# Performance work log

Measured on AMD Instinct MI355X. Metric: run time of the kernel, lower is better.

Reference implementation:

```python
import jax, jax.numpy as jnp
import numpy as np

ALPHA = 0.2  # LeakyReLU negative slope


def setup_inputs() -> dict:
    key = jax.random.key(0)
    k1, k2, k3, k4 = jax.random.split(key, 4)
    B, N, F_in, F_out = 2, 512, 256, 128
    x = jax.random.normal(k1, (B, N, F_in), dtype=jnp.float32)
    adj = jax.random.randint(k2, (B, N, N), 0, 2, dtype=jnp.int32)
    # xavier_uniform with gain=1.414 for W (in_features, out_features)
    limit = 1.414 * np.sqrt(6.0 / (F_in + F_out))
    W = jax.random.uniform(k3, (F_in, F_out), dtype=jnp.float32, minval=-limit, maxval=limit)
    # attn_fc: Linear(out_features, 1, bias=False); store its weight as a vector
    lim_a = np.sqrt(1.0 / F_out)
    a_fc = jax.random.uniform(k4, (F_out,), dtype=jnp.float32, minval=-lim_a, maxval=lim_a)
    return {"x": x, "adj": adj, "W": W, "a_fc": a_fc}


def reference(x, adj, W, a_fc):
    # x: [B,N,F_in], adj: [B,N,N], W: [F_in,F_out], a_fc: [F_out]
    Wh = jnp.einsum('bnf,fo->bno', x, W)                         # [B,N,O]
    s = Wh[:, :, None, :] + Wh[:, None, :, :]                    # [B,N,N,O] broadcast concat-sum
    e = jnp.einsum('bijo,o->bij', jax.nn.leaky_relu(s, ALPHA), a_fc)  # attn_fc -> [B,N,N]
    e = e / jnp.sqrt(jnp.sum(e * e))                             # torch.linalg.norm over whole tensor
    e = jnp.where(adj == 0, -jnp.inf, e)
    attention = jax.nn.softmax(e, axis=-1)
    h_prime = jnp.einsum('bij,bjo->bio', attention, Wh)          # [B,N,O]
    return jax.nn.elu(h_prime)                                   # concat=True -> elu
```

## Files before the change

kernel.cpp:

```cpp
#include <hip/hip_runtime.h>
#include <math.h>

constexpr int BB   = 2;
constexpr int NN   = 512;
constexpr int FIN  = 256;
constexpr int FOUT = 128;

__global__ __launch_bounds__(256) void wh_u_kernel(const float* __restrict__ x,
                                                   const float* __restrict__ W,
                                                   const float* __restrict__ a_fc,
                                                   float* __restrict__ Wh,
                                                   float* __restrict__ u2) {
    __shared__ float  xs[4 * FIN];
    __shared__ float4 part[4][16][17];

    const int t  = threadIdx.x;
    const int rg = blockIdx.x & 255;
    const int oh = blockIdx.x >> 8;
    const int g0 = rg * 4;

    ((float4*)xs)[t] = ((const float4*)(x + (size_t)g0 * FIN))[t];
    __syncthreads();

    const int og = t & 15;
    const int fs = t >> 4;
    const float* xr = xs + fs * 16;
    const float4* W4 = (const float4*)W;
    const int ob = oh * 16 + og;

    float4 a0 = {0.f,0.f,0.f,0.f}, a1 = {0.f,0.f,0.f,0.f};
    float4 a2 = {0.f,0.f,0.f,0.f}, a3 = {0.f,0.f,0.f,0.f};
#pragma unroll
    for (int f = 0; f < 16; ++f) {
        const float4 wv = W4[(size_t)(fs * 16 + f) * 32 + ob];
        const float v0 = xr[f];
        const float v1 = xr[FIN + f];
        const float v2 = xr[2 * FIN + f];
        const float v3 = xr[3 * FIN + f];
        a0.x = fmaf(v0, wv.x, a0.x); a1.x = fmaf(v1, wv.x, a1.x);
        a2.x = fmaf(v2, wv.x, a2.x); a3.x = fmaf(v3, wv.x, a3.x);
        a0.y = fmaf(v0, wv.y, a0.y); a1.y = fmaf(v1, wv.y, a1.y);
        a2.y = fmaf(v2, wv.y, a2.y); a3.y = fmaf(v3, wv.y, a3.y);
        a0.z = fmaf(v0, wv.z, a0.z); a1.z = fmaf(v1, wv.z, a1.z);
        a2.z = fmaf(v2, wv.z, a2.z); a3.z = fmaf(v3, wv.z, a3.z);
        a0.w = fmaf(v0, wv.w, a0.w); a1.w = fmaf(v1, wv.w, a1.w);
        a2.w = fmaf(v2, wv.w, a2.w); a3.w = fmaf(v3, wv.w, a3.w);
    }
    part[0][fs][og] = a0;
    part[1][fs][og] = a1;
    part[2][fs][og] = a2;
    part[3][fs][og] = a3;
    __syncthreads();

    if (t < 64) {
        const int rl = t >> 4;
        const int o4 = t & 15;
        float4 s = {0.f, 0.f, 0.f, 0.f};
#pragma unroll
        for (int k = 0; k < 16; ++k) {
            const float4 pk = part[rl][k][o4];
            s.x += pk.x; s.y += pk.y; s.z += pk.z; s.w += pk.w;
        }
        ((float4*)(Wh + (size_t)(g0 + rl) * FOUT))[oh * 16 + o4] = s;

        const float4 a4 = ((const float4*)a_fc)[oh * 16 + o4];
        float pa = s.x * a4.x + s.y * a4.y + s.z * a4.z + s.w * a4.w;
        pa += __shfl_down(pa, 8, 16);
        pa += __shfl_down(pa, 4, 16);
        pa += __shfl_down(pa, 2, 16);
        pa += __shfl_down(pa, 1, 16);
        if (o4 == 0) u2[(size_t)oh * 1024 + g0 + rl] = pa;
    }
}

__global__ __launch_bounds__(256) void e_kernel(const float* __restrict__ Wh,
                                                const float* __restrict__ u2,
                                                const float* __restrict__ a_fc,
                                                float* __restrict__ e_buf,
                                                float* __restrict__ partials) {
    __shared__ float whi[32][132];
    __shared__ float whj[16][132];
    __shared__ float a2[FOUT];
    __shared__ float usi[32];
    __shared__ float usj[16];
    __shared__ float parts[16][4][33];
    __shared__ float red[4];

    const int t   = threadIdx.x;
    const int bj0 = blockIdx.x * 16;
    const int bi0 = blockIdx.y * 32;
    const int b   = blockIdx.z;
    const float* whb = Wh + (size_t)(b * NN) * FOUT;

#pragma unroll
    for (int it = 0; it < 4; ++it) {
        const int idx = it * 256 + t;
        const int row = idx >> 5, c4 = idx & 31;
        *(float4*)&whi[row][c4 * 4] =
            *(const float4*)(whb + (size_t)(bi0 + row) * FOUT + c4 * 4);
    }
#pragma unroll
    for (int it = 0; it < 2; ++it) {
        const int idx = it * 256 + t;
        const int row = idx >> 5, c4 = idx & 31;
        *(float4*)&whj[row][c4 * 4] =
            *(const float4*)(whb + (size_t)(bj0 + row) * FOUT + c4 * 4);
    }
    if (t < 32)
        usi[t] = u2[b * NN + bi0 + t] + u2[1024 + b * NN + bi0 + t];
    else if (t < 48)
        usj[t - 32] = u2[b * NN + bj0 + (t - 32)] +
                      u2[1024 + b * NN + bj0 + (t - 32)];
    else if (t >= 128)
        a2[t - 128] = 0.4f * a_fc[t - 128];
    __syncthreads();

    const int w    = t >> 6;
    const int lane = t & 63;
    const int i    = lane & 31;
    const int jh   = lane >> 5;
    const int ob   = w * 32;

    float4 iv[8], av[8];
#pragma unroll
    for (int k = 0; k < 8; ++k) {
        iv[k] = *(const float4*)&whi[i][ob + 4 * k];
        av[k] = *(const float4*)&a2[ob + 4 * k];
    }

#pragma unroll
    for (int jj = 0; jj < 8; ++jj) {
        const int j = jh * 8 + jj;
        float4 acc = {0.f, 0.f, 0.f, 0.f};
#pragma unroll
        for (int k = 0; k < 8; ++k) {
            const float4 jv = *(const float4*)&whj[j][ob + 4 * k];
            float s;
            s = iv[k].x + jv.x; acc.x = fmaf(av[k].x, fabsf(s), acc.x);
            s = iv[k].y + jv.y; acc.y = fmaf(av[k].y, fabsf(s), acc.y);
            s = iv[k].z + jv.z; acc.z = fmaf(av[k].z, fabsf(s), acc.z);
            s = iv[k].w + jv.w; acc.w = fmaf(av[k].w, fabsf(s), acc.w);
        }
        parts[j][w][i] = (acc.x + acc.y) + (acc.z + acc.w);
    }
    __syncthreads();

    const int ci = t >> 3;
    const int jp = (t & 7) * 2;
    const float ui = usi[ci];

    const float S0 = (parts[jp][0][ci] + parts[jp][1][ci]) +
                     (parts[jp][2][ci] + parts[jp][3][ci]);
    const float v0 = fmaf(0.6f, ui + usj[jp], S0);
    const float S1 = (parts[jp + 1][0][ci] + parts[jp + 1][1][ci]) +
                     (parts[jp + 1][2][ci] + parts[jp + 1][3][ci]);
    const float v1 = fmaf(0.6f, ui + usj[jp + 1], S1);
    float ss = fmaf(v0, v0, v1 * v1);

    float2 e2 = {v0, v1};
    *(float2*)&e_buf[(size_t)(b * NN + bi0 + ci) * NN + bj0 + jp] = e2;

#pragma unroll
    for (int off = 32; off; off >>= 1) ss += __shfl_down(ss, off);
    if ((t & 63) == 0) red[t >> 6] = ss;
    __syncthreads();
    if (t == 0)
        partials[(blockIdx.z * 16 + blockIdx.y) * 32 + blockIdx.x] =
            (red[0] + red[1]) + (red[2] + red[3]);
}

__global__ __launch_bounds__(256) void softmax_pv_kernel(
        const float* __restrict__ e_buf, const int* __restrict__ adj,
        const float* __restrict__ Wh, const float* __restrict__ partials,
        float* __restrict__ out) {
    __shared__ float p[4][NN];
    __shared__ float hb[8][4][32];
    __shared__ float red[4];
    __shared__ float rsv[4];

    const int t    = threadIdx.x;
    const int w    = t >> 6;
    const int lane = t & 63;

    float v = (partials[t] + partials[t + 256]) +
              (partials[t + 512] + partials[t + 768]);
#pragma unroll
    for (int off = 32; off; off >>= 1) v += __shfl_down(v, off);
    if (lane == 0) red[w] = v;
    __syncthreads();
    const float inv_norm = 1.0f / sqrtf((red[0] + red[1]) + (red[2] + red[3]));

    const int g0  = (blockIdx.x & 255) * 4;
    const int oq  = blockIdx.x >> 8;
    const int row = g0 + w;

    const float4* er4 = (const float4*)(e_buf + (size_t)row * NN);
    const int4*   ad4 = (const int4*)(adj + (size_t)row * NN);
    const float4 ea = er4[lane],     eb = er4[lane + 64];
    const int4   aa = ad4[lane],     ab = ad4[lane + 64];

    float va[8];
    va[0] = aa.x ? ea.x * inv_norm : -INFINITY;
    va[1] = aa.y ? ea.y * inv_norm : -INFINITY;
    va[2] = aa.z ? ea.z * inv_norm : -INFINITY;
    va[3] = aa.w ? ea.w * inv_norm : -INFINITY;
    va[4] = ab.x ? eb.x * inv_norm : -INFINITY;
    va[5] = ab.y ? eb.y * inv_norm : -INFINITY;
    va[6] = ab.z ? eb.z * inv_norm : -INFINITY;
    va[7] = ab.w ? eb.w * inv_norm : -INFINITY;

    float mx = va[0];
#pragma unroll
    for (int c = 1; c < 8; ++c) mx = fmaxf(mx, va[c]);
#pragma unroll
    for (int off = 32; off; off >>= 1) mx = fmaxf(mx, __shfl_xor(mx, off));

    float pv[8], sum = 0.f;
#pragma unroll
    for (int c = 0; c < 8; ++c) { pv[c] = expf(va[c] - mx); sum += pv[c]; }
    float4 pa = {pv[0], pv[1], pv[2], pv[3]};
    float4 pb = {pv[4], pv[5], pv[6], pv[7]};
    ((float4*)&p[w][0])[lane]      = pa;
    ((float4*)&p[w][0])[lane + 64] = pb;

#pragma unroll
    for (int off = 32; off; off >>= 1) sum += __shfl_xor(sum, off);
    if (lane == 0) rsv[w] = 1.0f / sum;
    __syncthreads();

    const int oo = lane & 31;
    const int o  = oq * 32 + oo;
    const int jc = (w << 1) | (lane >> 5);
    const int b  = g0 >> 9;
    const float* whb = Wh + (size_t)(b * NN) * FOUT;
    const int j0 = jc * 64;

    float acc0 = 0.f, acc1 = 0.f, acc2 = 0.f, acc3 = 0.f;
    for (int j = j0; j < j0 + 64; j += 4) {
        const float4 p0 = *(const float4*)&p[0][j];
        const float4 p1 = *(const float4*)&p[1][j];
        const float4 p2 = *(const float4*)&p[2][j];
        const float4 p3 = *(const float4*)&p[3][j];
        float wv;
        wv = whb[(size_t)(j + 0) * FOUT + o];
        acc0 = fmaf(p0.x, wv, acc0); acc1 = fmaf(p1.x, wv, acc1);
        acc2 = fmaf(p2.x, wv, acc2); acc3 = fmaf(p3.x, wv, acc3);
        wv = whb[(size_t)(j + 1) * FOUT + o];
        acc0 = fmaf(p0.y, wv, acc0); acc1 = fmaf(p1.y, wv, acc1);
        acc2 = fmaf(p2.y, wv, acc2); acc3 = fmaf(p3.y, wv, acc3);
        wv = whb[(size_t)(j + 2) * FOUT + o];
        acc0 = fmaf(p0.z, wv, acc0); acc1 = fmaf(p1.z, wv, acc1);
        acc2 = fmaf(p2.z, wv, acc2); acc3 = fmaf(p3.z, wv, acc3);
        wv = whb[(size_t)(j + 3) * FOUT + o];
        acc0 = fmaf(p0.w, wv, acc0); acc1 = fmaf(p1.w, wv, acc1);
        acc2 = fmaf(p2.w, wv, acc2); acc3 = fmaf(p3.w, wv, acc3);
    }

    hb[jc][0][oo] = acc0;
    hb[jc][1][oo] = acc1;
    hb[jc][2][oo] = acc2;
    hb[jc][3][oo] = acc3;
    __syncthreads();

    if (t < 128) {
        const int r  = t >> 5;
        const int o2 = t & 31;
        float h = ((hb[0][r][o2] + hb[1][r][o2]) + (hb[2][r][o2] + hb[3][r][o2])) +
                  ((hb[4][r][o2] + hb[5][r][o2]) + (hb[6][r][o2] + hb[7][r][o2]));
        h *= rsv[r];
        out[(size_t)(g0 + r) * FOUT + oq * 32 + o2] = (h > 0.f) ? h : expm1f(h);
    }
}

extern "C" void kernel_launch(void* const* d_in, const int* in_sizes, int n_in,
                              void* d_out, int out_size, void* d_ws, size_t ws_size,
                              hipStream_t stream) {
    const float* x    = (const float*)d_in[0];
    const int*   adj  = (const int*)d_in[1];
    const float* W    = (const float*)d_in[2];
    const float* a_fc = (const float*)d_in[3];
    float* out = (float*)d_out;

    float* ws       = (float*)d_ws;
    float* Wh       = ws;
    float* u2       = ws + 131072;
    float* partials = ws + 131072 + 2048;
    float* e_buf    = ws + 131072 + 2048 + 1024;

    wh_u_kernel<<<dim3(512), dim3(256), 0, stream>>>(x, W, a_fc, Wh, u2);
    e_kernel<<<dim3(NN / 16, NN / 32, BB), dim3(256), 0, stream>>>(Wh, u2, a_fc, e_buf, partials);
    softmax_pv_kernel<<<dim3(1024), dim3(256), 0, stream>>>(e_buf, adj, Wh, partials, out);
}
```

Baseline: 24.63 us.

## Exploit symmetry of attention logits by computing only upper-triangular tiles

```diff
diff --git a/kernel.cpp b/kernel.cpp
--- a/kernel.cpp
+++ b/kernel.cpp
@@ -78,95 +78,94 @@
                                                 const float* __restrict__ a_fc,
                                                 float* __restrict__ e_buf,
                                                 float* __restrict__ partials) {
-    __shared__ float whi[32][132];
+    __shared__ float whi[16][132];
     __shared__ float whj[16][132];
-    __shared__ float a2[FOUT];
-    __shared__ float usi[32];
+    __shared__ float a2s[FOUT];
+    __shared__ float usi[16];
     __shared__ float usj[16];
-    __shared__ float parts[16][4][33];
+    __shared__ float parts[16][4][17];
     __shared__ float red[4];
 
-    const int t   = threadIdx.x;
-    const int bj0 = blockIdx.x * 16;
-    const int bi0 = blockIdx.y * 32;
-    const int b   = blockIdx.z;
+    const int t = threadIdx.x;
+    int s = blockIdx.x;
+    int b = 0;
+    if (s >= 528) { b = 1; s -= 528; }
+    int I = (int)(32.5f - sqrtf(1056.25f - 2.0f * (float)s));
+    int PI = 32 * I - (I * (I - 1)) / 2;
+    if (s < PI)                 { --I; PI = 32 * I - (I * (I - 1)) / 2; }
+    else if (s >= PI + 32 - I)  { PI += 32 - I; ++I; }
+    const int J    = I + (s - PI);
+    const int bi0  = I * 16, bj0 = J * 16;
+    const bool mir = (J > I);
+
     const float* whb = Wh + (size_t)(b * NN) * FOUT;
 
 #pragma unroll
-    for (int it = 0; it < 4; ++it) {
+    for (int it = 0; it < 2; ++it) {
         const int idx = it * 256 + t;
         const int row = idx >> 5, c4 = idx & 31;
         *(float4*)&whi[row][c4 * 4] =
             *(const float4*)(whb + (size_t)(bi0 + row) * FOUT + c4 * 4);
-    }
-#pragma unroll
-    for (int it = 0; it < 2; ++it) {
-        const int idx = it * 256 + t;
-        const int row = idx >> 5, c4 = idx & 31;
         *(float4*)&whj[row][c4 * 4] =
             *(const float4*)(whb + (size_t)(bj0 + row) * FOUT + c4 * 4);
     }
-    if (t < 32)
+    if (t < 16)
         usi[t] = u2[b * NN + bi0 + t] + u2[1024 + b * NN + bi0 + t];
-    else if (t < 48)
-        usj[t - 32] = u2[b * NN + bj0 + (t - 32)] +
-                      u2[1024 + b * NN + bj0 + (t - 32)];
+    else if (t < 32)
+        usj[t - 16] = u2[b * NN + bj0 + (t - 16)] +
+                      u2[1024 + b * NN + bj0 + (t - 16)];
     else if (t >= 128)
-        a2[t - 128] = 0.4f * a_fc[t - 128];
+        a2s[t - 128] = 0.4f * a_fc[t - 128];
     __syncthreads();
 
     const int w    = t >> 6;
     const int lane = t & 63;
-    const int i    = lane & 31;
-    const int jh   = lane >> 5;
+    const int i    = lane & 15;
+    const int jg   = lane >> 4;
     const int ob   = w * 32;
 
     float4 iv[8], av[8];
 #pragma unroll
     for (int k = 0; k < 8; ++k) {
         iv[k] = *(const float4*)&whi[i][ob + 4 * k];
-        av[k] = *(const float4*)&a2[ob + 4 * k];
-    }
-
-#pragma unroll
-    for (int jj = 0; jj < 8; ++jj) {
-        const int j = jh * 8 + jj;
+        av[k] = *(const float4*)&a2s[ob + 4 * k];
+    }
+
+#pragma unroll
+    for (int jj = 0; jj < 4; ++jj) {
+        const int j = jg * 4 + jj;
         float4 acc = {0.f, 0.f, 0.f, 0.f};
 #pragma unroll
         for (int k = 0; k < 8; ++k) {
             const float4 jv = *(const float4*)&whj[j][ob + 4 * k];
-            float s;
-            s = iv[k].x + jv.x; acc.x = fmaf(av[k].x, fabsf(s), acc.x);
-            s = iv[k].y + jv.y; acc.y = fmaf(av[k].y, fabsf(s), acc.y);
-            s = iv[k].z + jv.z; acc.z = fmaf(av[k].z, fabsf(s), acc.z);
-            s = iv[k].w + jv.w; acc.w = fmaf(av[k].w, fabsf(s), acc.w);
+            float sv;
+            sv = iv[k].x + jv.x; acc.x = fmaf(av[k].x, fabsf(sv), acc.x);
+            sv = iv[k].y + jv.y; acc.y = fmaf(av[k].y, fabsf(sv), acc.y);
+            sv = iv[k].z + jv.z; acc.z = fmaf(av[k].z, fabsf(sv), acc.z);
+            sv = iv[k].w + jv.w; acc.w = fmaf(av[k].w, fabsf(sv), acc.w);
         }
         parts[j][w][i] = (acc.x + acc.y) + (acc.z + acc.w);
     }
     __syncthreads();
 
-    const int ci = t >> 3;
-    const int jp = (t & 7) * 2;
-    const float ui = usi[ci];
-
-    const float S0 = (parts[jp][0][ci] + parts[jp][1][ci]) +
-                     (parts[jp][2][ci] + parts[jp][3][ci]);
-    const float v0 = fmaf(0.6f, ui + usj[jp], S0);
-    const float S1 = (parts[jp + 1][0][ci] + parts[jp + 1][1][ci]) +
-                     (parts[jp + 1][2][ci] + parts[jp + 1][3][ci]);
-    const float v1 = fmaf(0.6f, ui + usj[jp + 1], S1);
-    float ss = fmaf(v0, v0, v1 * v1);
-
-    float2 e2 = {v0, v1};
-    *(float2*)&e_buf[(size_t)(b * NN + bi0 + ci) * NN + bj0 + jp] = e2;
+    const int ci = t >> 4;
+    const int cj = t & 15;
+    const float S = (parts[cj][0][ci] + parts[cj][1][ci]) +
+                    (parts[cj][2][ci] + parts[cj][3][ci]);
+    const float v = fmaf(0.6f, usi[ci] + usj[cj], S);
+    float ss = v * v;
+    e_buf[(size_t)(b * NN + bi0 + ci) * NN + bj0 + cj] = v;
+    if (mir) {
+        e_buf[(size_t)(b * NN + bj0 + cj) * NN + bi0 + ci] = v;
+        ss += ss;
+    }
 
 #pragma unroll
     for (int off = 32; off; off >>= 1) ss += __shfl_down(ss, off);
     if ((t & 63) == 0) red[t >> 6] = ss;
     __syncthreads();
     if (t == 0)
-        partials[(blockIdx.z * 16 + blockIdx.y) * 32 + blockIdx.x] =
-            (red[0] + red[1]) + (red[2] + red[3]);
+        partials[blockIdx.x] = (red[0] + red[1]) + (red[2] + red[3]);
 }
 
 __global__ __launch_bounds__(256) void softmax_pv_kernel(
@@ -184,6 +183,7 @@
 
     float v = (partials[t] + partials[t + 256]) +
               (partials[t + 512] + partials[t + 768]);
+    if (t < 32) v += partials[t + 1024];
 #pragma unroll
     for (int off = 32; off; off >>= 1) v += __shfl_down(v, off);
     if (lane == 0) red[w] = v;
@@ -285,9 +285,9 @@
     float* Wh       = ws;
     float* u2       = ws + 131072;
     float* partials = ws + 131072 + 2048;
-    float* e_buf    = ws + 131072 + 2048 + 1024;
+    float* e_buf    = ws + 131072 + 2048 + 1280;
 
     wh_u_kernel<<<dim3(512), dim3(256), 0, stream>>>(x, W, a_fc, Wh, u2);
-    e_kernel<<<dim3(NN / 16, NN / 32, BB), dim3(256), 0, stream>>>(Wh, u2, a_fc, e_buf, partials);
+    e_kernel<<<dim3(1056), dim3(256), 0, stream>>>(Wh, u2, a_fc, e_buf, partials);
     softmax_pv_kernel<<<dim3(1024), dim3(256), 0, stream>>>(e_buf, adj, Wh, partials, out);
 }
```

After: 23.74 us, median of 2. -3.6%, faster.
